# Kernel tuning notes

Measured on AMD Instinct MI355X. Metric: run time of the kernel, lower is better.

Reference implementation:

```python
import jax, jax.numpy as jnp
import numpy as np

B, LQ, LK = 4, 256, 512
DQ, DK, DV = 512, 512, 512
H = 256
NEG = -1e6


def setup_inputs() -> dict:
    key = jax.random.key(0)
    ks = jax.random.split(key, 7)
    queries = jax.random.normal(ks[0], (B, LQ, DQ), dtype=jnp.float32)
    keys = jax.random.normal(ks[1], (B, LK, DK), dtype=jnp.float32)
    values = jax.random.normal(ks[2], (B, LK, DV), dtype=jnp.float32)
    valid_lens = jax.random.randint(ks[3], (B,), 1, LK + 1).astype(jnp.int32)
    # learned params (Linear without bias): store as (in, out) so x @ W matches torch x @ W.T
    Wq = jax.random.normal(ks[4], (DQ, H), dtype=jnp.float32) * (1.0 / np.sqrt(DQ))
    Wk = jax.random.normal(ks[5], (DK, H), dtype=jnp.float32) * (1.0 / np.sqrt(DK))
    wv = jax.random.normal(ks[6], (H,), dtype=jnp.float32) * (1.0 / np.sqrt(H))
    return {"queries": queries, "keys": keys, "values": values,
            "valid_lens": valid_lens, "Wq": Wq, "Wk": Wk, "wv": wv}


def reference(queries, keys, values, valid_lens, Wq, Wk, wv):
    q = jnp.einsum('bqd,dh->bqh', queries, Wq)          # (B,Lq,H)
    k = jnp.einsum('bkd,dh->bkh', keys, Wk)             # (B,Lk,H)
    feats = jnp.tanh(q[:, :, None, :] + k[:, None, :, :])  # (B,Lq,Lk,H)
    scores = jnp.einsum('bqkh,h->bqk', feats, wv)        # (B,Lq,Lk)
    mask = jnp.arange(LK)[None, None, :] < valid_lens[:, None, None]  # (B,1,Lk)
    attn = jax.nn.softmax(jnp.where(mask, scores, NEG), axis=-1)
    return jnp.einsum('bqk,bkv->bqv', attn, values)      # (B,Lq,Dv)
```

## Files before the change

kernel.cpp:

```cpp
#include <hip/hip_runtime.h>

#define B_   4
#define LQ_  256
#define LK_  512
#define DIN_ 512
#define H_   256
#define DV_  512

#define L2E 1.4426950408889634f

__global__ __launch_bounds__(256) void proj_partial_kernel(
    const float* __restrict__ Q, const float* __restrict__ K,
    const float* __restrict__ Wq, const float* __restrict__ Wk,
    const int* __restrict__ valid_lens,
    float* __restrict__ qpart, float* __restrict__ ekpart) {
  __shared__ float xs[64][68];
  __shared__ float ws[64][132];

  const int blk = blockIdx.x;
  const bool isQ = blk < 128;
  int b, row0, h0, ds;
  if (isQ) {
    const int qi = blk;
    ds = qi & 3; h0 = ((qi >> 2) & 1) * 128;
    const int rt = qi >> 3;
    b = rt >> 2; row0 = (rt & 3) * 64;
  } else {
    const int u = blk - 128;
    ds = u & 3; h0 = ((u >> 2) & 1) * 128;
    const int rt = u >> 3;
    b = rt & 3; row0 = (rt >> 2) * 64;
    if (row0 >= valid_lens[b]) return;
  }
  const int L = isQ ? LQ_ : LK_;
  const float* __restrict__ X = (isQ ? Q : K) + ((size_t)(b * L + row0)) * DIN_ + ds * 128;
  const float* __restrict__ Wb = (isQ ? Wq : Wk) + (size_t)(ds * 128) * H_ + h0;

  const int t = threadIdx.x;
  const int hthr = t & 31;
  const int rthr = t >> 5;

  float acc[8][4];
#pragma unroll
  for (int r = 0; r < 8; ++r)
#pragma unroll
    for (int c = 0; c < 4; ++c) acc[r][c] = 0.f;

  for (int dd = 0; dd < 128; dd += 64) {
    __syncthreads();
#pragma unroll
    for (int u = 0; u < 4; ++u) {
      const int f = t + 256 * u;
      const int r = f >> 4, c4 = (f & 15) << 2;
      *(float4*)&xs[r][c4] = *(const float4*)&X[(size_t)r * DIN_ + dd + c4];
    }
#pragma unroll
    for (int u = 0; u < 8; ++u) {
      const int f = t + 256 * u;
      const int k = f >> 5, c4 = (f & 31) << 2;
      *(float4*)&ws[k][c4] = *(const float4*)&Wb[(size_t)(dd + k) * H_ + c4];
    }
    __syncthreads();

    for (int k = 0; k < 64; k += 8) {
      float4 w4[8];
#pragma unroll
      for (int k8 = 0; k8 < 8; ++k8)
        w4[k8] = *(const float4*)&ws[k + k8][4 * hthr];
#pragma unroll
      for (int rr = 0; rr < 8; ++rr) {
        const float4 xa = *(const float4*)&xs[rthr * 8 + rr][k];
        const float4 xb = *(const float4*)&xs[rthr * 8 + rr][k + 4];
        const float xv[8] = {xa.x, xa.y, xa.z, xa.w, xb.x, xb.y, xb.z, xb.w};
#pragma unroll
        for (int k8 = 0; k8 < 8; ++k8) {
          acc[rr][0] = fmaf(xv[k8], w4[k8].x, acc[rr][0]);
          acc[rr][1] = fmaf(xv[k8], w4[k8].y, acc[rr][1]);
          acc[rr][2] = fmaf(xv[k8], w4[k8].z, acc[rr][2]);
          acc[rr][3] = fmaf(xv[k8], w4[k8].w, acc[rr][3]);
        }
      }
    }
  }

  float* dst = isQ ? (qpart + (size_t)ds * (B_ * LQ_ * H_))
                   : (ekpart + (size_t)ds * (B_ * LK_ * H_));
#pragma unroll
  for (int rr = 0; rr < 8; ++rr) {
    const int row = row0 + rthr * 8 + rr;
    float4 o = {acc[rr][0], acc[rr][1], acc[rr][2], acc[rr][3]};
    *(float4*)&dst[(size_t)(b * L + row) * H_ + h0 + 4 * hthr] = o;
  }
}

__global__ __launch_bounds__(512) void combine_exp_kernel(
    const float* __restrict__ qpart, const float* __restrict__ ekpart,
    const float* __restrict__ wv,
    float* __restrict__ eq, float* __restrict__ ek, float* __restrict__ wsum) {
  const int idx = blockIdx.x * 512 + threadIdx.x;
  const int NQ4 = B_ * LQ_ * H_ / 4;
  const float4* src;
  float4* dst;
  size_t stride4;
  int k4;
  if (idx < NQ4) {
    src = (const float4*)qpart; dst = (float4*)eq;
    stride4 = NQ4; k4 = idx;
  } else {
    src = (const float4*)ekpart; dst = (float4*)ek;
    stride4 = B_ * LK_ * H_ / 4; k4 = idx - NQ4;
  }
  float4 a = src[k4];
  float4 b1 = src[stride4 + k4];
  float4 c = src[2 * stride4 + k4];
  float4 d = src[3 * stride4 + k4];
  float4 o;
  o.x = exp2f(fminf(fmaxf((a.x + b1.x + c.x + d.x) * L2E, -126.f), 126.f));
  o.y = exp2f(fminf(fmaxf((a.y + b1.y + c.y + d.y) * L2E, -126.f), 126.f));
  o.z = exp2f(fminf(fmaxf((a.z + b1.z + c.z + d.z) * L2E, -126.f), 126.f));
  o.w = exp2f(fminf(fmaxf((a.w + b1.w + c.w + d.w) * L2E, -126.f), 126.f));
  dst[k4] = o;

  if (blockIdx.x == 0 && threadIdx.x < 64) {
    const int t = threadIdx.x;
    float s = wv[t] + wv[t + 64] + wv[t + 128] + wv[t + 192];
#pragma unroll
    for (int off = 32; off; off >>= 1) s += __shfl_xor(s, off);
    if (t == 0) *wsum = s;
  }
}

__global__ __launch_bounds__(256) void scores_kernel(
    const float* __restrict__ eq, const float* __restrict__ ek,
    const float* __restrict__ wv, const float* __restrict__ wsum,
    const int* __restrict__ valid_lens, float* __restrict__ sc) {
  __shared__ float eq_s[32][260];
  __shared__ float ek_s[256][36];
  __shared__ float wv_s[260];

  const int blk = blockIdx.x;
  const int b  = blk & 3;
  const int it = (blk >> 2) & 7;
  const int jt = blk >> 5;
  const int vl = valid_lens[b];
  if (jt * 32 >= vl) return;
  const int t = threadIdx.x;
  const int tx = t & 15, ty = t >> 4;
  const int i0 = it * 32, j0 = jt * 32;

  const float* __restrict__ eqb = eq + ((size_t)(b * LQ_ + i0)) * H_;
#pragma unroll
  for (int u = 0; u < 8; ++u) {
    const int f = t + 256 * u;
    const int r = f >> 6, c4 = (f & 63) << 2;
    *(float4*)&eq_s[r][c4] = *(const float4*)&eqb[(size_t)r * H_ + c4];
  }
  const float* __restrict__ ekb = ek + ((size_t)(b * LK_ + j0)) * H_;
  {
    const int hq = t & 63, jg = t >> 6;
#pragma unroll
    for (int p = 0; p < 8; ++p) {
      const int jj = jg + 4 * p;
      const float4 v = *(const float4*)&ekb[(size_t)jj * H_ + 4 * hq];
      ek_s[4 * hq][jj]     = v.x;
      ek_s[4 * hq + 1][jj] = v.y;
      ek_s[4 * hq + 2][jj] = v.z;
      ek_s[4 * hq + 3][jj] = v.w;
    }
  }
  if (t < 64) {
#pragma unroll
    for (int u = 0; u < 4; ++u) wv_s[t + 64 * u] = wv[t + 64 * u];
  }
  __syncthreads();

  const float Wsum = *wsum;
  float a00 = 0.f, a01 = 0.f, a10 = 0.f, a11 = 0.f;
#pragma unroll 2
  for (int hq = 0; hq < 64; ++hq) {
    const float4 q0 = *(const float4*)&eq_s[2 * ty][4 * hq];
    const float4 q1 = *(const float4*)&eq_s[2 * ty + 1][4 * hq];
    const float4 w4 = *(const float4*)&wv_s[4 * hq];
    const float qa[4] = {q0.x, q0.y, q0.z, q0.w};
    const float qb[4] = {q1.x, q1.y, q1.z, q1.w};
    const float ww[4] = {w4.x, w4.y, w4.z, w4.w};
#pragma unroll
    for (int u = 0; u < 4; ++u) {
      const float2 kk = *(const float2*)&ek_s[4 * hq + u][2 * tx];
      float p;
      p = qa[u] * kk.x; a00 = fmaf(ww[u], __builtin_amdgcn_rcpf(fmaf(p, p, 1.f)), a00);
      p = qa[u] * kk.y; a01 = fmaf(ww[u], __builtin_amdgcn_rcpf(fmaf(p, p, 1.f)), a01);
      p = qb[u] * kk.x; a10 = fmaf(ww[u], __builtin_amdgcn_rcpf(fmaf(p, p, 1.f)), a10);
      p = qb[u] * kk.y; a11 = fmaf(ww[u], __builtin_amdgcn_rcpf(fmaf(p, p, 1.f)), a11);
    }
  }
  const int i = i0 + 2 * ty, j = j0 + 2 * tx;
  float2 r0 = {fmaf(-2.f, a00, Wsum), fmaf(-2.f, a01, Wsum)};
  float2 r1 = {fmaf(-2.f, a10, Wsum), fmaf(-2.f, a11, Wsum)};
  *(float2*)&sc[(size_t)(b * LQ_ + i) * LK_ + j] = r0;
  *(float2*)&sc[(size_t)(b * LQ_ + i + 1) * LK_ + j] = r1;
}

__global__ __launch_bounds__(512) void softmax_av_kernel(
    const float* __restrict__ sc, const float* __restrict__ V,
    const int* __restrict__ valid_lens, float* __restrict__ out) {
  __shared__ float4 p4s[LK_];
  __shared__ float redm[8][4];
  __shared__ float reds[8][4];

  const int blk = blockIdx.x;
  const int b = blk >> 6;
  const int i0 = (blk & 63) * 4;
  const int vl = valid_lens[b];
  const int t = threadIdx.x;
  const int lane = t & 63, wave = t >> 6;

  const float* __restrict__ srow = sc + (size_t)(b * LQ_ + i0) * LK_;
  const bool valid = t < vl;
  float s[4], m[4];
#pragma unroll
  for (int ii = 0; ii < 4; ++ii) {
    s[ii] = valid ? srow[ii * LK_ + t] : -3.0e38f;
    m[ii] = s[ii];
  }
#pragma unroll
  for (int off = 32; off; off >>= 1)
#pragma unroll
    for (int ii = 0; ii < 4; ++ii) m[ii] = fmaxf(m[ii], __shfl_xor(m[ii], off));
  if (lane == 0)
#pragma unroll
    for (int ii = 0; ii < 4; ++ii) redm[wave][ii] = m[ii];
  __syncthreads();
  float e[4], sum[4];
#pragma unroll
  for (int ii = 0; ii < 4; ++ii) {
    float mx = redm[0][ii];
#pragma unroll
    for (int w = 1; w < 8; ++w) mx = fmaxf(mx, redm[w][ii]);
    e[ii] = valid ? __expf(s[ii] - mx) : 0.f;
    sum[ii] = e[ii];
  }
#pragma unroll
  for (int off = 32; off; off >>= 1)
#pragma unroll
    for (int ii = 0; ii < 4; ++ii) sum[ii] += __shfl_xor(sum[ii], off);
  if (lane == 0)
#pragma unroll
    for (int ii = 0; ii < 4; ++ii) reds[wave][ii] = sum[ii];
  __syncthreads();
  {
    float4 pv;
    float tot[4];
#pragma unroll
    for (int ii = 0; ii < 4; ++ii) {
      tot[ii] = reds[0][ii];
#pragma unroll
      for (int w = 1; w < 8; ++w) tot[ii] += reds[w][ii];
    }
    pv.x = e[0] * __builtin_amdgcn_rcpf(tot[0]);
    pv.y = e[1] * __builtin_amdgcn_rcpf(tot[1]);
    pv.z = e[2] * __builtin_amdgcn_rcpf(tot[2]);
    pv.w = e[3] * __builtin_amdgcn_rcpf(tot[3]);
    p4s[t] = pv;
  }
  __syncthreads();

  const float* __restrict__ Vb = V + (size_t)b * LK_ * DV_ + t;
  float a[4] = {0.f, 0.f, 0.f, 0.f};
  int j = 0;
  const int jv = vl & ~7;
  for (; j < jv; j += 8) {
    float v[8];
#pragma unroll
    for (int u = 0; u < 8; ++u) v[u] = Vb[(size_t)(j + u) * DV_];
#pragma unroll
    for (int u = 0; u < 8; ++u) {
      const float4 pp = p4s[j + u];
      a[0] = fmaf(pp.x, v[u], a[0]); a[1] = fmaf(pp.y, v[u], a[1]);
      a[2] = fmaf(pp.z, v[u], a[2]); a[3] = fmaf(pp.w, v[u], a[3]);
    }
  }
  for (; j < vl; ++j) {
    const float v = Vb[(size_t)j * DV_];
    const float4 pp = p4s[j];
    a[0] = fmaf(pp.x, v, a[0]); a[1] = fmaf(pp.y, v, a[1]);
    a[2] = fmaf(pp.z, v, a[2]); a[3] = fmaf(pp.w, v, a[3]);
  }
#pragma unroll
  for (int ii = 0; ii < 4; ++ii)
    out[(size_t)(b * LQ_ + i0 + ii) * DV_ + t] = a[ii];
}

extern "C" void kernel_launch(void* const* d_in, const int* in_sizes, int n_in,
                              void* d_out, int out_size, void* d_ws, size_t ws_size,
                              hipStream_t stream) {
  const float* queries    = (const float*)d_in[0];
  const float* keys       = (const float*)d_in[1];
  const float* values     = (const float*)d_in[2];
  const int*   valid_lens = (const int*)d_in[3];
  const float* Wq         = (const float*)d_in[4];
  const float* Wk         = (const float*)d_in[5];
  const float* wv         = (const float*)d_in[6];
  float* out = (float*)d_out;

  char* ws = (char*)d_ws;
  float* qpart  = (float*)ws;
  float* ekpart = (float*)(ws + (size_t)( 4 << 20));
  float* eq     = (float*)(ws + (size_t)(12 << 20));
  float* ek     = (float*)(ws + (size_t)(13 << 20));
  float* sc     = (float*)(ws + (size_t)(15 << 20));
  float* wsum   = (float*)(ws + (size_t)(17 << 20));

  proj_partial_kernel<<<384, 256, 0, stream>>>(
      queries, keys, Wq, Wk, valid_lens, qpart, ekpart);
  combine_exp_kernel<<<384, 512, 0, stream>>>(
      qpart, ekpart, wv, eq, ek, wsum);
  scores_kernel<<<512, 256, 0, stream>>>(
      eq, ek, wv, wsum, valid_lens, sc);
  softmax_av_kernel<<<B_ * (LQ_ / 4), 512, 0, stream>>>(
      sc, values, valid_lens, out);
}
```

Baseline: 62.72 us.

## Retile projection kernel to 16-row blocks with direct weight loads; pad ek_s to 33

New measurement: 63.71 us. About the same (+1.6%).

```diff
diff --git a/kernel.cpp b/kernel.cpp
--- a/kernel.cpp
+++ b/kernel.cpp
@@ -14,83 +14,60 @@
     const float* __restrict__ Wq, const float* __restrict__ Wk,
     const int* __restrict__ valid_lens,
     float* __restrict__ qpart, float* __restrict__ ekpart) {
-  __shared__ float xs[64][68];
-  __shared__ float ws[64][132];
-
+  __shared__ float xs[16][132];
   const int blk = blockIdx.x;
-  const bool isQ = blk < 128;
-  int b, row0, h0, ds;
+  const bool isQ = blk < 256;
+  int flat, ds;
   if (isQ) {
-    const int qi = blk;
-    ds = qi & 3; h0 = ((qi >> 2) & 1) * 128;
-    const int rt = qi >> 3;
-    b = rt >> 2; row0 = (rt & 3) * 64;
+    const int u = blk;
+    ds = u & 3;
+    flat = (u >> 2) * 16;
   } else {
-    const int u = blk - 128;
-    ds = u & 3; h0 = ((u >> 2) & 1) * 128;
-    const int rt = u >> 3;
-    b = rt & 3; row0 = (rt >> 2) * 64;
-    if (row0 >= valid_lens[b]) return;
-  }
-  const int L = isQ ? LQ_ : LK_;
-  const float* __restrict__ X = (isQ ? Q : K) + ((size_t)(b * L + row0)) * DIN_ + ds * 128;
-  const float* __restrict__ Wb = (isQ ? Wq : Wk) + (size_t)(ds * 128) * H_ + h0;
-
+    const int u = blk - 256;
+    ds = u & 3;
+    const int rt = u >> 2;
+    const int b = rt & 3;
+    const int rl = (rt >> 2) * 16;
+    if (rl >= valid_lens[b]) return;
+    flat = b * LK_ + rl;
+  }
+  const float* __restrict__ X = (isQ ? Q : K) + (size_t)flat * DIN_ + ds * 128;
+  const float* __restrict__ W = (isQ ? Wq : Wk) + (size_t)(ds * 128) * H_;
   const int t = threadIdx.x;
-  const int hthr = t & 31;
-  const int rthr = t >> 5;
-
-  float acc[8][4];
-#pragma unroll
-  for (int r = 0; r < 8; ++r)
-#pragma unroll
-    for (int c = 0; c < 4; ++c) acc[r][c] = 0.f;
-
-  for (int dd = 0; dd < 128; dd += 64) {
-    __syncthreads();
-#pragma unroll
-    for (int u = 0; u < 4; ++u) {
-      const int f = t + 256 * u;
-      const int r = f >> 4, c4 = (f & 15) << 2;
-      *(float4*)&xs[r][c4] = *(const float4*)&X[(size_t)r * DIN_ + dd + c4];
-    }
-#pragma unroll
-    for (int u = 0; u < 8; ++u) {
-      const int f = t + 256 * u;
-      const int k = f >> 5, c4 = (f & 31) << 2;
-      *(float4*)&ws[k][c4] = *(const float4*)&Wb[(size_t)(dd + k) * H_ + c4];
-    }
-    __syncthreads();
-
-    for (int k = 0; k < 64; k += 8) {
-      float4 w4[8];
-#pragma unroll
-      for (int k8 = 0; k8 < 8; ++k8)
-        w4[k8] = *(const float4*)&ws[k + k8][4 * hthr];
-#pragma unroll
-      for (int rr = 0; rr < 8; ++rr) {
-        const float4 xa = *(const float4*)&xs[rthr * 8 + rr][k];
-        const float4 xb = *(const float4*)&xs[rthr * 8 + rr][k + 4];
-        const float xv[8] = {xa.x, xa.y, xa.z, xa.w, xb.x, xb.y, xb.z, xb.w};
-#pragma unroll
-        for (int k8 = 0; k8 < 8; ++k8) {
-          acc[rr][0] = fmaf(xv[k8], w4[k8].x, acc[rr][0]);
-          acc[rr][1] = fmaf(xv[k8], w4[k8].y, acc[rr][1]);
-          acc[rr][2] = fmaf(xv[k8], w4[k8].z, acc[rr][2]);
-          acc[rr][3] = fmaf(xv[k8], w4[k8].w, acc[rr][3]);
-        }
-      }
-    }
-  }
-
-  float* dst = isQ ? (qpart + (size_t)ds * (B_ * LQ_ * H_))
-                   : (ekpart + (size_t)ds * (B_ * LK_ * H_));
-#pragma unroll
-  for (int rr = 0; rr < 8; ++rr) {
-    const int row = row0 + rthr * 8 + rr;
-    float4 o = {acc[rr][0], acc[rr][1], acc[rr][2], acc[rr][3]};
-    *(float4*)&dst[(size_t)(b * L + row) * H_ + h0 + 4 * hthr] = o;
-  }
+
+#pragma unroll
+  for (int u = 0; u < 2; ++u) {
+    const int f = t + 256 * u;
+    const int r = f >> 5, c4 = (f & 31) << 2;
+    *(float4*)&xs[r][c4] = *(const float4*)&X[(size_t)r * DIN_ + c4];
+  }
+  __syncthreads();
+
+  float acc[16];
+#pragma unroll
+  for (int r = 0; r < 16; ++r) acc[r] = 0.f;
+
+  for (int d = 0; d < 128; d += 8) {
+    float w[8];
+#pragma unroll
+    for (int u = 0; u < 8; ++u)
+      w[u] = W[(size_t)(d + u) * H_ + t];
+#pragma unroll
+    for (int r = 0; r < 16; ++r) {
+      const float4 xa = *(const float4*)&xs[r][d];
+      const float4 xb = *(const float4*)&xs[r][d + 4];
+      acc[r] = fmaf(xa.x, w[0], acc[r]); acc[r] = fmaf(xa.y, w[1], acc[r]);
+      acc[r] = fmaf(xa.z, w[2], acc[r]); acc[r] = fmaf(xa.w, w[3], acc[r]);
+      acc[r] = fmaf(xb.x, w[4], acc[r]); acc[r] = fmaf(xb.y, w[5], acc[r]);
+      acc[r] = fmaf(xb.z, w[6], acc[r]); acc[r] = fmaf(xb.w, w[7], acc[r]);
+    }
+  }
+
+  float* __restrict__ dst = isQ ? (qpart + (size_t)ds * (B_ * LQ_ * H_))
+                                : (ekpart + (size_t)ds * (B_ * LK_ * H_));
+#pragma unroll
+  for (int r = 0; r < 16; ++r)
+    dst[(size_t)(flat + r) * H_ + t] = acc[r];
 }
 
 __global__ __launch_bounds__(512) void combine_exp_kernel(
@@ -135,7 +112,7 @@
     const float* __restrict__ wv, const float* __restrict__ wsum,
     const int* __restrict__ valid_lens, float* __restrict__ sc) {
   __shared__ float eq_s[32][260];
-  __shared__ float ek_s[256][36];
+  __shared__ float ek_s[256][33];
   __shared__ float wv_s[260];
 
   const int blk = blockIdx.x;
@@ -186,12 +163,13 @@
     const float ww[4] = {w4.x, w4.y, w4.z, w4.w};
 #pragma unroll
     for (int u = 0; u < 4; ++u) {
-      const float2 kk = *(const float2*)&ek_s[4 * hq + u][2 * tx];
+      const float kx = ek_s[4 * hq + u][2 * tx];
+      const float ky = ek_s[4 * hq + u][2 * tx + 1];
       float p;
-      p = qa[u] * kk.x; a00 = fmaf(ww[u], __builtin_amdgcn_rcpf(fmaf(p, p, 1.f)), a00);
-      p = qa[u] * kk.y; a01 = fmaf(ww[u], __builtin_amdgcn_rcpf(fmaf(p, p, 1.f)), a01);
-      p = qb[u] * kk.x; a10 = fmaf(ww[u], __builtin_amdgcn_rcpf(fmaf(p, p, 1.f)), a10);
-      p = qb[u] * kk.y; a11 = fmaf(ww[u], __builtin_amdgcn_rcpf(fmaf(p, p, 1.f)), a11);
+      p = qa[u] * kx; a00 = fmaf(ww[u], __builtin_amdgcn_rcpf(fmaf(p, p, 1.f)), a00);
+      p = qa[u] * ky; a01 = fmaf(ww[u], __builtin_amdgcn_rcpf(fmaf(p, p, 1.f)), a01);
+      p = qb[u] * kx; a10 = fmaf(ww[u], __builtin_amdgcn_rcpf(fmaf(p, p, 1.f)), a10);
+      p = qb[u] * ky; a11 = fmaf(ww[u], __builtin_amdgcn_rcpf(fmaf(p, p, 1.f)), a11);
     }
   }
   const int i = i0 + 2 * ty, j = j0 + 2 * tx;
@@ -311,7 +289,7 @@
   float* sc     = (float*)(ws + (size_t)(15 << 20));
   float* wsum   = (float*)(ws + (size_t)(17 << 20));
 
-  proj_partial_kernel<<<384, 256, 0, stream>>>(
+  proj_partial_kernel<<<768, 256, 0, stream>>>(
       queries, keys, Wq, Wk, valid_lens, qpart, ekpart);
   combine_exp_kernel<<<384, 512, 0, stream>>>(
       qpart, ekpart, wv, eq, ek, wsum);
```
